# Kernel optimization log

Measured on AMD Instinct MI355X. Metric: run time of the kernel, lower is better.

Reference implementation:

```python
import jax, jax.numpy as jnp
import numpy as np

REDUCTION_SIZE = 2


def setup_inputs() -> dict:
    key = jax.random.key(0)
    k1, k2 = jax.random.split(key)
    T, E, K, D = 32768, 256, 8, 8  # tokens, experts, top-k, devices
    topk_tensor = jax.random.normal(k1, (1, 1, T, E), dtype=jnp.float32)
    # one-hot expert -> device mapping (contiguous blocks of E//D experts per device)
    dev_of_expert = jnp.arange(E, dtype=jnp.int32) // (E // D)
    expert_mapping = jax.nn.one_hot(dev_of_expert, D, dtype=jnp.int32)[None, None]  # [1,1,E,D]
    expert_metadata = jax.random.randint(k2, (1, 1, T, K), 0, E, dtype=jnp.int32)[None][0]
    return {
        "topk_tensor": topk_tensor,
        "expert_mapping": expert_mapping,
        "expert_metadata": expert_metadata,
    }


def reference(topk_tensor, expert_mapping, expert_metadata):
    r = REDUCTION_SIZE
    topk = topk_tensor[0, 0]          # [T, E] scores over all experts
    mapping = expert_mapping[0, 0]    # [E, D] one-hot expert->device
    meta = expert_metadata[0, 0]      # [T, K] selected expert indices
    T, E = topk.shape
    D = mapping.shape[-1]

    dev_of_expert = jnp.argmax(mapping, axis=-1)            # [E]
    tok_dev = dev_of_expert[meta]                           # [T, K] device of each selected expert

    # token -> device dispatch mask, reduced over groups of `r` tokens
    rows = jnp.arange(T, dtype=jnp.int32)[:, None]
    mask = jnp.zeros((T, D), dtype=jnp.int32).at[rows, tok_dev].set(1)  # [T, D]
    reduced_mask = mask.reshape(T // r, r, D).max(axis=1)               # [T//r, D]

    # selection mask over experts (scatter, avoids [T,K,E] one-hot blowup)
    sel = jnp.zeros((T, E), dtype=topk.dtype).at[rows, meta].set(1.0)   # [T, E]
    gated = topk * sel                                                  # zero non-selected scores

    # remap expert columns into device-local slots
    perm = jnp.argsort(dev_of_expert, stable=True)                      # experts grouped by device
    remapped = gated[:, perm].reshape(T, D, E // D).transpose(1, 0, 2)  # [D, T, E//D]
    return remapped, reduced_mask
```

## Files before the change

kernel.cpp:

```cpp
#include <hip/hip_runtime.h>

#define T_TOK 32768
#define E_EXP 256
#define K_SEL 8
#define D_DEV 8
#define SLOTS (E_EXP / D_DEV)

__global__ void moe_setup_kernel(const int* __restrict__ mapping,
                                 int* __restrict__ dev_out,
                                 int* __restrict__ pos_out) {
    __shared__ int sdev[E_EXP];
    int e = threadIdx.x;
    int best = mapping[e * D_DEV];
    int dev = 0;
#pragma unroll
    for (int d = 1; d < D_DEV; ++d) {
        int v = mapping[e * D_DEV + d];
        if (v > best) { best = v; dev = d; }
    }
    sdev[e] = dev;
    __syncthreads();
    int p = 0;
    for (int e2 = 0; e2 < E_EXP; ++e2) {
        int d2 = sdev[e2];
        p += (d2 < dev) || (d2 == dev && e2 < e);
    }
    dev_out[e] = dev;
    pos_out[e] = p;
}

__global__ __launch_bounds__(256) void moe_remap_kernel(
    const float* __restrict__ topk, const int* __restrict__ meta,
    const int* __restrict__ dev_of_expert, const int* __restrict__ pos,
    float* __restrict__ out_remap, float* __restrict__ out_mask) {
    __shared__ unsigned int sdm[4];

    const int tid  = threadIdx.x;
    const int wave = tid >> 6;
    const int lane = tid & 63;
    const int t    = blockIdx.x * 4 + wave;

    const int4* mp = (const int4*)(meta + (size_t)t * K_SEL);
    int4 m01 = mp[0];
    int4 m23 = mp[1];
    int mv[8] = {m01.x, m01.y, m01.z, m01.w, m23.x, m23.y, m23.z, m23.w};

    unsigned sel = 0;
#pragma unroll
    for (int k = 0; k < K_SEL; ++k) {
        sel |= ((mv[k] >> 2) == lane) ? (1u << (mv[k] & 3)) : 0u;
    }

    if (lane == 0) {
        unsigned dm = 0;
#pragma unroll
        for (int k = 0; k < K_SEL; ++k) dm |= 1u << dev_of_expert[mv[k]];
        sdm[wave] = dm;
    }

    float4 v = *(const float4*)(topk + (size_t)t * E_EXP + lane * 4);
    v.x = (sel & 1u) ? v.x : 0.0f;
    v.y = (sel & 2u) ? v.y : 0.0f;
    v.z = (sel & 4u) ? v.z : 0.0f;
    v.w = (sel & 8u) ? v.w : 0.0f;

    int4 p4 = *(const int4*)(pos + lane * 4);
    if (p4.y == p4.x + 1 && p4.z == p4.x + 2 && p4.w == p4.x + 3 &&
        (p4.x & 3) == 0) {
        const int d = p4.x >> 5, j = p4.x & 31;
        *(float4*)(out_remap + (size_t)d * T_TOK * SLOTS + (size_t)t * SLOTS + j) = v;
    } else {
        float vv[4] = {v.x, v.y, v.z, v.w};
        int   pp[4] = {p4.x, p4.y, p4.z, p4.w};
#pragma unroll
        for (int i = 0; i < 4; ++i) {
            out_remap[(size_t)(pp[i] >> 5) * T_TOK * SLOTS + (size_t)t * SLOTS +
                      (pp[i] & 31)] = vv[i];
        }
    }

    __syncthreads();
    if (tid < 16) {
        const int pair = tid >> 3, d = tid & 7;
        const unsigned dm = sdm[pair * 2] | sdm[pair * 2 + 1];
        const int row = (blockIdx.x * 4) / 2 + pair;
        out_mask[(size_t)row * D_DEV + d] = ((dm >> d) & 1u) ? 1.0f : 0.0f;
    }
}

extern "C" void kernel_launch(void* const* d_in, const int* in_sizes, int n_in,
                              void* d_out, int out_size, void* d_ws, size_t ws_size,
                              hipStream_t stream) {
    const float* topk    = (const float*)d_in[0];
    const int*   mapping = (const int*)d_in[1];
    const int*   meta    = (const int*)d_in[2];

    float* out_remap = (float*)d_out;
    float* out_mask  = out_remap + (size_t)D_DEV * T_TOK * SLOTS;

    int* dev_ws = (int*)d_ws;
    int* pos_ws = dev_ws + E_EXP;

    moe_setup_kernel<<<1, 256, 0, stream>>>(mapping, dev_ws, pos_ws);
    moe_remap_kernel<<<T_TOK / 4, 256, 0, stream>>>(topk, meta, dev_ws, pos_ws,
                                                    out_remap, out_mask);
}
```

Measured before the change: 94.59 us.

## Fuse setup into remap kernel and gather only selected topk scores

```diff
diff --git a/kernel.cpp b/kernel.cpp
--- a/kernel.cpp
+++ b/kernel.cpp
@@ -5,103 +5,122 @@
 #define K_SEL 8
 #define D_DEV 8
 #define SLOTS (E_EXP / D_DEV)
+#define NBLK  1024
+#define TOK_PER_BLK (T_TOK / NBLK)
+#define PAIRS_PER_WAVE (TOK_PER_BLK / 2 / 4)
 
-__global__ void moe_setup_kernel(const int* __restrict__ mapping,
-                                 int* __restrict__ dev_out,
-                                 int* __restrict__ pos_out) {
-    __shared__ int sdev[E_EXP];
-    int e = threadIdx.x;
-    int best = mapping[e * D_DEV];
-    int dev = 0;
+__global__ __launch_bounds__(256) void moe_fused_kernel(
+    const float* __restrict__ topk, const int* __restrict__ mapping,
+    const int* __restrict__ meta, float* __restrict__ out_remap,
+    float* __restrict__ out_mask) {
+  __shared__ int sdev[E_EXP];
+  __shared__ int spos[E_EXP];
+  __shared__ int scnt[4 * D_DEV];
+
+  const int tid  = threadIdx.x;
+  const int w    = tid >> 6;
+  const int lane = tid & 63;
+
+  {
+    const int e = tid;
+    int4 m0 = ((const int4*)mapping)[e * 2];
+    int4 m1 = ((const int4*)mapping)[e * 2 + 1];
+    int vals[8] = {m0.x, m0.y, m0.z, m0.w, m1.x, m1.y, m1.z, m1.w};
+    int best = vals[0], dev = 0;
 #pragma unroll
-    for (int d = 1; d < D_DEV; ++d) {
-        int v = mapping[e * D_DEV + d];
-        if (v > best) { best = v; dev = d; }
+    for (int d = 1; d < 8; ++d)
+      if (vals[d] > best) { best = vals[d]; dev = d; }
+    sdev[e] = dev;
+
+    unsigned long long myball = 0ull;
+#pragma unroll
+    for (int d = 0; d < 8; ++d) {
+      unsigned long long b = __ballot(dev == d);
+      if (d == dev) myball = b;
+      if (lane == d) scnt[w * 8 + d] = __popcll(b);
     }
-    sdev[e] = dev;
+    const unsigned long long lt =
+        (lane == 0) ? 0ull : (~0ull >> (64 - lane));
+    const int lower = __popcll(myball & lt);
     __syncthreads();
-    int p = 0;
-    for (int e2 = 0; e2 < E_EXP; ++e2) {
-        int d2 = sdev[e2];
-        p += (d2 < dev) || (d2 == dev && e2 < e);
-    }
-    dev_out[e] = dev;
-    pos_out[e] = p;
-}
+    int base = 0;
+    for (int d = 0; d < dev; ++d)
+      base += scnt[0 * 8 + d] + scnt[1 * 8 + d] + scnt[2 * 8 + d] +
+              scnt[3 * 8 + d];
+    for (int w2 = 0; w2 < w; ++w2) base += scnt[w2 * 8 + dev];
+    spos[e] = base + lower;
+    __syncthreads();
+  }
 
-__global__ __launch_bounds__(256) void moe_remap_kernel(
-    const float* __restrict__ topk, const int* __restrict__ meta,
-    const int* __restrict__ dev_of_expert, const int* __restrict__ pos,
-    float* __restrict__ out_remap, float* __restrict__ out_mask) {
-    __shared__ unsigned int sdm[4];
+  const int e0 = lane * 4;
+  const int p0 = spos[e0], p1 = spos[e0 + 1], p2 = spos[e0 + 2],
+            p3 = spos[e0 + 3];
+  const bool contig =
+      (p1 == p0 + 1) && (p2 == p0 + 2) && (p3 == p0 + 3) && ((p0 & 3) == 0);
+  float* const contig_base =
+      out_remap + (size_t)(p0 >> 5) * T_TOK * SLOTS + (p0 & 31);
 
-    const int tid  = threadIdx.x;
-    const int wave = tid >> 6;
-    const int lane = tid & 63;
-    const int t    = blockIdx.x * 4 + wave;
+  const int tok_base = blockIdx.x * TOK_PER_BLK;
 
-    const int4* mp = (const int4*)(meta + (size_t)t * K_SEL);
-    int4 m01 = mp[0];
-    int4 m23 = mp[1];
-    int mv[8] = {m01.x, m01.y, m01.z, m01.w, m23.x, m23.y, m23.z, m23.w};
+#pragma unroll
+  for (int j = 0; j < PAIRS_PER_WAVE; ++j) {
+    const int pair = w + 4 * j;
+    const int t0 = tok_base + 2 * pair;
+    unsigned dmask = 0;
 
-    unsigned sel = 0;
 #pragma unroll
-    for (int k = 0; k < K_SEL; ++k) {
-        sel |= ((mv[k] >> 2) == lane) ? (1u << (mv[k] & 3)) : 0u;
+    for (int s = 0; s < 2; ++s) {
+      const int t = t0 + s;
+      const int4* mp = (const int4*)(meta + (size_t)t * K_SEL);
+      int4 a = mp[0], b = mp[1];
+      int mv[8] = {a.x, a.y, a.z, a.w, b.x, b.y, b.z, b.w};
+
+      float4 v = {0.f, 0.f, 0.f, 0.f};
+      const float* row = topk + (size_t)t * E_EXP;
+#pragma unroll
+      for (int k = 0; k < K_SEL; ++k) {
+        const int e = mv[k];
+        dmask |= 1u << sdev[e];
+        if ((e >> 2) == lane) {
+          const float x = row[e];
+          const int slot = e & 3;
+          if (slot == 0) v.x = x;
+          else if (slot == 1) v.y = x;
+          else if (slot == 2) v.z = x;
+          else v.w = x;
+        }
+      }
+
+      if (contig) {
+        *(float4*)(contig_base + (size_t)t * SLOTS) = v;
+      } else {
+        float vv[4] = {v.x, v.y, v.z, v.w};
+        int pp[4] = {p0, p1, p2, p3};
+#pragma unroll
+        for (int i = 0; i < 4; ++i)
+          out_remap[(size_t)(pp[i] >> 5) * T_TOK * SLOTS + (size_t)t * SLOTS +
+                    (pp[i] & 31)] = vv[i];
+      }
     }
 
-    if (lane == 0) {
-        unsigned dm = 0;
-#pragma unroll
-        for (int k = 0; k < K_SEL; ++k) dm |= 1u << dev_of_expert[mv[k]];
-        sdm[wave] = dm;
+    if (lane < 8) {
+      const int rowi = t0 >> 1;
+      out_mask[(size_t)rowi * D_DEV + lane] =
+          ((dmask >> lane) & 1u) ? 1.0f : 0.0f;
     }
-
-    float4 v = *(const float4*)(topk + (size_t)t * E_EXP + lane * 4);
-    v.x = (sel & 1u) ? v.x : 0.0f;
-    v.y = (sel & 2u) ? v.y : 0.0f;
-    v.z = (sel & 4u) ? v.z : 0.0f;
-    v.w = (sel & 8u) ? v.w : 0.0f;
-
-    int4 p4 = *(const int4*)(pos + lane * 4);
-    if (p4.y == p4.x + 1 && p4.z == p4.x + 2 && p4.w == p4.x + 3 &&
-        (p4.x & 3) == 0) {
-        const int d = p4.x >> 5, j = p4.x & 31;
-        *(float4*)(out_remap + (size_t)d * T_TOK * SLOTS + (size_t)t * SLOTS + j) = v;
-    } else {
-        float vv[4] = {v.x, v.y, v.z, v.w};
-        int   pp[4] = {p4.x, p4.y, p4.z, p4.w};
-#pragma unroll
-        for (int i = 0; i < 4; ++i) {
-            out_remap[(size_t)(pp[i] >> 5) * T_TOK * SLOTS + (size_t)t * SLOTS +
-                      (pp[i] & 31)] = vv[i];
-        }
-    }
-
-    __syncthreads();
-    if (tid < 16) {
-        const int pair = tid >> 3, d = tid & 7;
-        const unsigned dm = sdm[pair * 2] | sdm[pair * 2 + 1];
-        const int row = (blockIdx.x * 4) / 2 + pair;
-        out_mask[(size_t)row * D_DEV + d] = ((dm >> d) & 1u) ? 1.0f : 0.0f;
-    }
+  }
 }
 
 extern "C" void kernel_launch(void* const* d_in, const int* in_sizes, int n_in,
                               void* d_out, int out_size, void* d_ws, size_t ws_size,
                               hipStream_t stream) {
-    const float* topk    = (const float*)d_in[0];
-    const int*   mapping = (const int*)d_in[1];
-    const int*   meta    = (const int*)d_in[2];
+  const float* topk    = (const float*)d_in[0];
+  const int*   mapping = (const int*)d_in[1];
+  const int*   meta    = (const int*)d_in[2];
 
-    float* out_remap = (float*)d_out;
-    float* out_mask  = out_remap + (size_t)D_DEV * T_TOK * SLOTS;
+  float* out_remap = (float*)d_out;
+  float* out_mask  = out_remap + (size_t)D_DEV * T_TOK * SLOTS;
 
-    int* dev_ws = (int*)d_ws;
-    int* pos_ws = dev_ws + E_EXP;
-
-    moe_setup_kernel<<<1, 256, 0, stream>>>(mapping, dev_ws, pos_ws);
-    moe_remap_kernel<<<T_TOK / 4, 256, 0, stream>>>(topk, meta, dev_ws, pos_ws,
-                                                    out_remap, out_mask);
+  moe_fused_kernel<<<NBLK, 256, 0, stream>>>(topk, mapping, meta, out_remap,
+                                             out_mask);
 }
```

Result: slower. 115.8 us (+22.5%).
